# Kernel tuning notes

Measured on AMD Instinct MI355X. Metric: run time of the kernel, lower is better.

## Reference

```python
import jax, jax.numpy as jnp
import numpy as np

N_USERS = 50000
N_ENT = 150000
N = N_USERS + N_ENT
E = 2000000
B = 8192
DIMS = [64, 64, 32, 16]  # emb_dim + weight_size


def _xavier(k, shape):
    fi, fo = (shape[0], shape[1]) if len(shape) == 2 else (1, shape[-1])
    lim = float(np.sqrt(6.0 / (fi + fo)))
    return jax.random.uniform(k, shape, jnp.float32, -lim, lim)


def setup_inputs() -> dict:
    key = jax.random.key(0)
    ks = jax.random.split(key, 32)
    inp = {}
    inp["users"] = jax.random.randint(ks[0], (B,), 0, N_USERS)
    inp["pos_items"] = jax.random.randint(ks[1], (B,), 0, N_ENT)
    inp["neg_items"] = jax.random.randint(ks[2], (B,), 0, N_ENT)
    inp["rows"] = jax.random.randint(ks[3], (E,), 0, N)
    inp["cols"] = jax.random.randint(ks[4], (E,), 0, N)
    # attentive normalized adjacency values (softmax-normalized in KGAT, ~1/degree scale)
    inp["edge_vals"] = jax.random.uniform(ks[5], (E,), jnp.float32) / 10.0
    inp["user_embed"] = _xavier(ks[6], (N_USERS, DIMS[0]))
    inp["entity_embed"] = _xavier(ks[7], (N_ENT, DIMS[0]))
    i = 8
    for l in range(3):
        din, dout = DIMS[l], DIMS[l + 1]
        inp[f"W_gc{l}"] = _xavier(ks[i], (din, dout)); i += 1
        inp[f"b_gc{l}"] = _xavier(ks[i], (1, dout)); i += 1
        inp[f"W_bi{l}"] = _xavier(ks[i], (din, dout)); i += 1
        inp[f"b_bi{l}"] = _xavier(ks[i], (1, dout)); i += 1
    return inp


def _l2norm(x):
    # F.normalize(x, p=2, dim=1)
    return x / jnp.maximum(jnp.linalg.norm(x, axis=1, keepdims=True), 1e-12)


def reference(users, pos_items, neg_items, rows, cols, edge_vals, user_embed, entity_embed,
              W_gc0, b_gc0, W_bi0, b_bi0, W_gc1, b_gc1, W_bi1, b_bi1, W_gc2, b_gc2, W_bi2, b_bi2):
    ego = jnp.concatenate([user_embed, entity_embed], axis=0)  # [N, 64]
    layer_params = [(W_gc0, b_gc0, W_bi0, b_bi0),
                    (W_gc1, b_gc1, W_bi1, b_bi1),
                    (W_gc2, b_gc2, W_bi2, b_bi2)]
    embs = [ego]
    for Wg, bg, Wb, bb in layer_params:
        # side = A_in @ ego  (sparse COO matmul as gather + segment_sum)
        side = jax.ops.segment_sum(edge_vals[:, None] * ego[cols], rows, num_segments=N)
        sum_emb = jax.nn.leaky_relu((ego + side) @ Wg + bg)  # bi-interaction sum branch
        bi_emb = jax.nn.leaky_relu((ego * side) @ Wb + bb)   # bi-interaction elementwise branch
        ego = sum_emb + bi_emb
        embs.append(_l2norm(ego))
    all_emb = jnp.concatenate(embs, axis=1)  # [N, 64+64+32+16]
    ua, ea = all_emb[:N_USERS], all_emb[N_USERS:]
    u_e = ua[users]
    pos_i_e = ea[pos_items]
    neg_i_e = ea[neg_items]
    pos_scores = jnp.sum(u_e * pos_i_e, axis=1)
    neg_scores = jnp.sum(u_e * neg_i_e, axis=1)
    return jnp.stack([pos_scores, neg_scores], axis=-1)  # [B, 2]
```

## Files before the change

kernel.cpp:

```cpp
#include <hip/hip_runtime.h>

#define N_USERS 50000
#define N_ENT   150000
#define N_NODES 200000
#define NE      2000000
#define BATCH   8192

#define BSHIFT 9
#define BROWS  512
#define NBUK   391
#define EPB    4096
#define PBLK   489
#define T0_BLKS 12500
#define WT_BLKS 52

typedef __attribute__((ext_vector_type(8))) short   bf16x8;
typedef __attribute__((ext_vector_type(4))) float   f32x4;

__device__ __forceinline__ float bf2f(unsigned short b) {
    return __uint_as_float(((unsigned int)b) << 16);
}
__device__ __forceinline__ unsigned short f2bf(float f) {
    unsigned int u = __float_as_uint(f);
    u += 0x7FFF + ((u >> 16) & 1);
    return (unsigned short)(u >> 16);
}

__global__ __launch_bounds__(256) void bhist(const int4* __restrict__ rows4,
                                             int* __restrict__ bcnt) {
    __shared__ int lcnt[NBUK];
    for (int b = threadIdx.x; b < NBUK; b += 256) lcnt[b] = 0;
    __syncthreads();
    const int q0 = blockIdx.x * (EPB / 4);
#pragma unroll
    for (int k = 0; k < 4; ++k) {
        int q = q0 + k * 256 + threadIdx.x;
        if (q < NE / 4) {
            int4 r = rows4[q];
            atomicAdd(&lcnt[r.x >> BSHIFT], 1);
            atomicAdd(&lcnt[r.y >> BSHIFT], 1);
            atomicAdd(&lcnt[r.z >> BSHIFT], 1);
            atomicAdd(&lcnt[r.w >> BSHIFT], 1);
        }
    }
    __syncthreads();
    for (int b = threadIdx.x; b < NBUK; b += 256) {
        int c = lcnt[b];
        if (c) atomicAdd(&bcnt[b], c);
    }
}

__global__ __launch_bounds__(512) void bscan(const int* __restrict__ bcnt,
                                             int* __restrict__ bsc,
                                             int* __restrict__ gcur) {
    __shared__ int buf[512];
    int t = threadIdx.x;
    int v = (t < NBUK) ? bcnt[t] : 0;
    buf[t] = v;
    __syncthreads();
    for (int off = 1; off < 512; off <<= 1) {
        int x = (t >= off) ? buf[t - off] : 0;
        __syncthreads();
        buf[t] += x;
        __syncthreads();
    }
    if (t < NBUK) {
        int excl = buf[t] - v;
        bsc[t]  = excl;
        gcur[t] = excl;
    }
    if (t == NBUK - 1) bsc[NBUK] = buf[t];
}

__global__ __launch_bounds__(256) void part_kernel(const int4* __restrict__ rows4,
                                                   const int4* __restrict__ cols4,
                                                   const float4* __restrict__ vals4,
                                                   int* __restrict__ gcur,
                                                   uint2* __restrict__ part) {
    __shared__ int lcnt[NBUK];
    __shared__ int lbase[NBUK];
    for (int b = threadIdx.x; b < NBUK; b += 256) lcnt[b] = 0;
    __syncthreads();
    const int q0 = blockIdx.x * (EPB / 4);
    int4 rc[4];
#pragma unroll
    for (int k = 0; k < 4; ++k) {
        int q = q0 + k * 256 + threadIdx.x;
        if (q < NE / 4) {
            int4 r = rows4[q];
            rc[k] = r;
            atomicAdd(&lcnt[r.x >> BSHIFT], 1);
            atomicAdd(&lcnt[r.y >> BSHIFT], 1);
            atomicAdd(&lcnt[r.z >> BSHIFT], 1);
            atomicAdd(&lcnt[r.w >> BSHIFT], 1);
        } else {
            rc[k] = make_int4(-1, -1, -1, -1);
        }
    }
    __syncthreads();
    for (int b = threadIdx.x; b < NBUK; b += 256) {
        int c = lcnt[b];
        lbase[b] = c ? atomicAdd(&gcur[b], c) : 0;
        lcnt[b] = 0;
    }
    __syncthreads();
#pragma unroll
    for (int k = 0; k < 4; ++k) {
        int q = q0 + k * 256 + threadIdx.x;
        if (q < NE / 4) {
            int4   c4 = cols4[q];
            float4 v4 = vals4[q];
            int r, b, rk;
            uint2 rec;
            r = rc[k].x; b = r >> BSHIFT; rk = atomicAdd(&lcnt[b], 1);
            rec.x = ((unsigned)(r & (BROWS - 1)) << 18) | (unsigned)c4.x;
            rec.y = __float_as_uint(v4.x);  part[lbase[b] + rk] = rec;
            r = rc[k].y; b = r >> BSHIFT; rk = atomicAdd(&lcnt[b], 1);
            rec.x = ((unsigned)(r & (BROWS - 1)) << 18) | (unsigned)c4.y;
            rec.y = __float_as_uint(v4.y);  part[lbase[b] + rk] = rec;
            r = rc[k].z; b = r >> BSHIFT; rk = atomicAdd(&lcnt[b], 1);
            rec.x = ((unsigned)(r & (BROWS - 1)) << 18) | (unsigned)c4.z;
            rec.y = __float_as_uint(v4.z);  part[lbase[b] + rk] = rec;
            r = rc[k].w; b = r >> BSHIFT; rk = atomicAdd(&lcnt[b], 1);
            rec.x = ((unsigned)(r & (BROWS - 1)) << 18) | (unsigned)c4.w;
            rec.y = __float_as_uint(v4.w);  part[lbase[b] + rk] = rec;
        }
    }
}

__global__ __launch_bounds__(512) void bfill(const uint2* __restrict__ part,
                                             const int* __restrict__ bsc,
                                             int* __restrict__ rs,
                                             int* __restrict__ deg,
                                             uint2* __restrict__ ep) {
    __shared__ int h[BROWS];
    __shared__ int sc[BROWS];
    const int b = blockIdx.x;
    const int t = threadIdx.x;
    const int s = bsc[b];
    const int e = bsc[b + 1];
    h[t] = 0;
    __syncthreads();
    for (int i = s + t; i < e; i += 512)
        atomicAdd(&h[part[i].x >> 18], 1);
    __syncthreads();
    int v = h[t];
    sc[t] = v;
    __syncthreads();
    for (int off = 1; off < 512; off <<= 1) {
        int x = (t >= off) ? sc[t - off] : 0;
        __syncthreads();
        sc[t] += x;
        __syncthreads();
    }
    const int row = b * BROWS + t;
    if (row < N_NODES) {
        deg[row] = v;
        rs[row]  = s + sc[t];
    }
    h[t] = s + sc[t] - v;
    __syncthreads();
    for (int i = s + t; i < e; i += 512) {
        uint2 rec = part[i];
        int lr  = rec.x >> 18;
        int pos = atomicAdd(&h[lr], 1);
        uint2 o;
        o.x = rec.x & 0x3FFFF;
        o.y = rec.y;
        ep[pos] = o;
    }
}

__global__ __launch_bounds__(256) void init_misc(
        const float* __restrict__ ue, const float* __restrict__ ee,
        unsigned short* __restrict__ t0,
        const float* __restrict__ Wg0, const float* __restrict__ Wb0,
        const float* __restrict__ Wg1, const float* __restrict__ Wb1,
        const float* __restrict__ Wg2, const float* __restrict__ Wb2,
        unsigned short* __restrict__ wt) {
    if (blockIdx.x < T0_BLKS) {
        int i = blockIdx.x * 256 + threadIdx.x;
        const int uelems = N_USERS * 64 / 4;
        float4 v = (i < uelems) ? ((const float4*)ue)[i]
                                : ((const float4*)ee)[i - uelems];
        ushort4 o;
        o.x = f2bf(v.x); o.y = f2bf(v.y); o.z = f2bf(v.z); o.w = f2bf(v.w);
        ((ushort4*)t0)[i] = o;
        return;
    }
    int idx = (blockIdx.x - T0_BLKS) * 256 + threadIdx.x;
    if (idx < 4096) {
        int k = idx >> 6, n = idx & 63;
        wt[0 + n * 64 + k] = f2bf(Wg0[idx]);
    } else if (idx < 8192) {
        int r = idx - 4096; int k = r >> 6, n = r & 63;
        wt[4096 + n * 64 + k] = f2bf(Wb0[r]);
    } else if (idx < 10240) {
        int r = idx - 8192; int k = r >> 5, n = r & 31;
        wt[8192 + n * 64 + k] = f2bf(Wg1[r]);
    } else if (idx < 12288) {
        int r = idx - 10240; int k = r >> 5, n = r & 31;
        wt[10240 + n * 64 + k] = f2bf(Wb1[r]);
    } else if (idx < 12800) {
        int r = idx - 12288; int k = r >> 4, n = r & 15;
        wt[12288 + n * 32 + k] = f2bf(Wg2[r]);
    } else if (idx < 13312) {
        int r = idx - 12800; int k = r >> 4, n = r & 15;
        wt[12800 + n * 32 + k] = f2bf(Wb2[r]);
    }
}

template <int DIN, int DOUT, int EGO, int WX>
__global__ __launch_bounds__(256) void layer_fused(
        const int* __restrict__ rs, const int* __restrict__ deg,
        const uint2* __restrict__ ep,
        const unsigned short* __restrict__ tin,
        const float* __restrict__ ue, const float* __restrict__ ee,
        const float* __restrict__ xin,
        const unsigned short* __restrict__ WgT,
        const unsigned short* __restrict__ WbT,
        const float* __restrict__ bg, const float* __restrict__ bb,
        float* __restrict__ xout,
        unsigned short* __restrict__ tout,
        float* __restrict__ norm_out) {
    constexpr int NTC = DOUT / 16;
    constexpr int R   = (4 / NTC) * 16;
    constexpr int RPW = R / 4;
    constexpr int KS  = DIN / 32;

    __shared__ unsigned short sH[R * DIN];
    __shared__ unsigned short sP[R * DIN];
    __shared__ float sPart[R * NTC];

    const int lane    = threadIdx.x & 63;
    const int wave    = threadIdx.x >> 6;
    const int rowbase = blockIdx.x * R;

    for (int rr = 0; rr < RPW; ++rr) {
        const int lr  = wave * RPW + rr;
        const int row = __builtin_amdgcn_readfirstlane(rowbase + lr);
        const int end   = rs[row];
        const int start = end - deg[row];

        float acc;
        if (DIN == 64) {
            float a0 = 0.f, a1 = 0.f, a2 = 0.f, a3 = 0.f;
            for (int i = start; i < end; i += 4) {
                uint2 r0 = ep[i + 0], r1 = ep[i + 1];
                uint2 r2 = ep[i + 2], r3 = ep[i + 3];
                int c0 = (int)r0.x;
                int c1 = ((unsigned)r1.x < N_NODES) ? (int)r1.x : 0;
                int c2 = ((unsigned)r2.x < N_NODES) ? (int)r2.x : 0;
                int c3 = ((unsigned)r3.x < N_NODES) ? (int)r3.x : 0;
                float v0 = __uint_as_float(r0.y);
                float v1 = (i + 1 < end) ? __uint_as_float(r1.y) : 0.f;
                float v2 = (i + 2 < end) ? __uint_as_float(r2.y) : 0.f;
                float v3 = (i + 3 < end) ? __uint_as_float(r3.y) : 0.f;
                a0 = fmaf(v0, bf2f(tin[(size_t)c0 * 64 + lane]), a0);
                a1 = fmaf(v1, bf2f(tin[(size_t)c1 * 64 + lane]), a1);
                a2 = fmaf(v2, bf2f(tin[(size_t)c2 * 64 + lane]), a2);
                a3 = fmaf(v3, bf2f(tin[(size_t)c3 * 64 + lane]), a3);
            }
            acc = (a0 + a1) + (a2 + a3);
        } else {
            const int g = lane >> 5;
            const int d = lane & 31;
            float a0 = 0.f, a1 = 0.f, a2 = 0.f, a3 = 0.f;
            for (int i = start; i < end; i += 8) {
                uint2 r0 = ep[i + 0], r1 = ep[i + 1], r2 = ep[i + 2], r3 = ep[i + 3];
                uint2 r4 = ep[i + 4], r5 = ep[i + 5], r6 = ep[i + 6], r7 = ep[i + 7];
                int c0 = (int)r0.x;
                int c1 = ((unsigned)r1.x < N_NODES) ? (int)r1.x : 0;
                int c2 = ((unsigned)r2.x < N_NODES) ? (int)r2.x : 0;
                int c3 = ((unsigned)r3.x < N_NODES) ? (int)r3.x : 0;
                int c4 = ((unsigned)r4.x < N_NODES) ? (int)r4.x : 0;
                int c5 = ((unsigned)r5.x < N_NODES) ? (int)r5.x : 0;
                int c6 = ((unsigned)r6.x < N_NODES) ? (int)r6.x : 0;
                int c7 = ((unsigned)r7.x < N_NODES) ? (int)r7.x : 0;
                float v0 = __uint_as_float(r0.y);
                float v1 = (i + 1 < end) ? __uint_as_float(r1.y) : 0.f;
                float v2 = (i + 2 < end) ? __uint_as_float(r2.y) : 0.f;
                float v3 = (i + 3 < end) ? __uint_as_float(r3.y) : 0.f;
                float v4 = (i + 4 < end) ? __uint_as_float(r4.y) : 0.f;
                float v5 = (i + 5 < end) ? __uint_as_float(r5.y) : 0.f;
                float v6 = (i + 6 < end) ? __uint_as_float(r6.y) : 0.f;
                float v7 = (i + 7 < end) ? __uint_as_float(r7.y) : 0.f;
                int   ca = g ? c4 : c0;  float va = g ? v4 : v0;
                int   cb = g ? c5 : c1;  float vb = g ? v5 : v1;
                int   cc = g ? c6 : c2;  float vc = g ? v6 : v2;
                int   cd = g ? c7 : c3;  float vd = g ? v7 : v3;
                a0 = fmaf(va, bf2f(tin[(size_t)ca * 32 + d]), a0);
                a1 = fmaf(vb, bf2f(tin[(size_t)cb * 32 + d]), a1);
                a2 = fmaf(vc, bf2f(tin[(size_t)cc * 32 + d]), a2);
                a3 = fmaf(vd, bf2f(tin[(size_t)cd * 32 + d]), a3);
            }
            acc = (a0 + a1) + (a2 + a3);
            acc += __shfl_xor(acc, 32);
        }

        const int d = (DIN == 64) ? lane : (lane & 31);
        float e;
        if (EGO == 0) {
            e = (row < N_USERS) ? ue[(size_t)row * 64 + lane]
                                : ee[(size_t)(row - N_USERS) * 64 + lane];
        } else if (EGO == 1) {
            e = xin[(size_t)row * DIN + lane];
        } else {
            e = bf2f(tin[(size_t)row * DIN + d]);
        }
        float h = e + acc;
        float p = e * acc;
        if (DIN == 64 || lane < 32) {
            sH[lr * DIN + d] = f2bf(h);
            sP[lr * DIN + d] = f2bf(p);
        }
    }
    __syncthreads();

    const int ct  = wave % NTC;
    const int rt  = wave / NTC;
    const int r16 = lane & 15;
    const int g4  = lane >> 4;

    bf16x8 ah[KS], ap[KS];
#pragma unroll
    for (int s = 0; s < KS; ++s) {
        const int aoff = (rt * 16 + r16) * DIN + g4 * 8 + s * 32;
        ah[s] = *reinterpret_cast<const bf16x8*>(sH + aoff);
        ap[s] = *reinterpret_cast<const bf16x8*>(sP + aoff);
    }
    f32x4 accg = (f32x4){0.f, 0.f, 0.f, 0.f};
    f32x4 accb = (f32x4){0.f, 0.f, 0.f, 0.f};
#pragma unroll
    for (int s = 0; s < KS; ++s) {
        const int boff = (ct * 16 + r16) * DIN + g4 * 8 + s * 32;
        bf16x8 bgf = *reinterpret_cast<const bf16x8*>(WgT + boff);
        bf16x8 bbf = *reinterpret_cast<const bf16x8*>(WbT + boff);
        accg = __builtin_amdgcn_mfma_f32_16x16x32_bf16(ah[s], bgf, accg, 0, 0, 0);
        accb = __builtin_amdgcn_mfma_f32_16x16x32_bf16(ap[s], bbf, accb, 0, 0, 0);
    }

    const int col = ct * 16 + r16;
    const float bgv = bg[col];
    const float bbv = bb[col];
    float ss[4];
#pragma unroll
    for (int r = 0; r < 4; ++r) {
        float a = accg[r] + bgv; a = a > 0.f ? a : 0.01f * a;
        float b = accb[r] + bbv; b = b > 0.f ? b : 0.01f * b;
        float nv = a + b;
        const int row = rowbase + rt * 16 + g4 * 4 + r;
        if (WX) xout[(size_t)row * DOUT + col] = nv;
        tout[(size_t)row * DOUT + col] = f2bf(nv);
        ss[r] = nv * nv;
    }
#pragma unroll
    for (int off = 1; off < 16; off <<= 1) {
#pragma unroll
        for (int r = 0; r < 4; ++r) ss[r] += __shfl_xor(ss[r], off);
    }
    if (r16 == 0) {
#pragma unroll
        for (int r = 0; r < 4; ++r)
            sPart[(rt * 16 + g4 * 4 + r) * NTC + ct] = ss[r];
    }
    __syncthreads();
    for (int t = threadIdx.x; t < R; t += 256) {
        float s = 0.f;
#pragma unroll
        for (int j = 0; j < NTC; ++j) s += sPart[t * NTC + j];
        norm_out[rowbase + t] = fmaxf(sqrtf(s), 1e-12f);
    }
}

__global__ __launch_bounds__(256) void score_kernel(
        const int* __restrict__ users, const int* __restrict__ pos,
        const int* __restrict__ neg,
        const float* __restrict__ ue, const float* __restrict__ ee,
        const float* __restrict__ e1, const float* __restrict__ n0,
        const unsigned short* __restrict__ t2, const float* __restrict__ n1,
        const unsigned short* __restrict__ t3, const float* __restrict__ n2,
        float* __restrict__ out) {
    int gid  = blockIdx.x * 256 + threadIdx.x;
    int idx  = gid >> 6;
    int lane = gid & 63;
    if (idx >= BATCH) return;
    int u  = users[idx];
    int pe = pos[idx];
    int ne = neg[idx];
    int pn = N_USERS + pe;
    int nn = N_USERS + ne;

    float s1p = 1.0f / (n0[u] * n0[pn]);
    float s1n = 1.0f / (n0[u] * n0[nn]);
    float s2p = 1.0f / (n1[u] * n1[pn]);
    float s2n = 1.0f / (n1[u] * n1[nn]);
    float s3p = 1.0f / (n2[u] * n2[pn]);
    float s3n = 1.0f / (n2[u] * n2[nn]);

    float ap = 0.f, an = 0.f;
    {
        float xu = ue[(size_t)u * 64 + lane];
        ap += xu * ee[(size_t)pe * 64 + lane];
        an += xu * ee[(size_t)ne * 64 + lane];
    }
    {
        float xu = e1[(size_t)u * 64 + lane];
        ap += xu * e1[(size_t)pn * 64 + lane] * s1p;
        an += xu * e1[(size_t)nn * 64 + lane] * s1n;
    }
    if (lane < 32) {
        float xu = bf2f(t2[(size_t)u * 32 + lane]);
        ap += xu * bf2f(t2[(size_t)pn * 32 + lane]) * s2p;
        an += xu * bf2f(t2[(size_t)nn * 32 + lane]) * s2n;
    } else if (lane < 48) {
        int d = lane - 32;
        float xu = bf2f(t3[(size_t)u * 16 + d]);
        ap += xu * bf2f(t3[(size_t)pn * 16 + d]) * s3p;
        an += xu * bf2f(t3[(size_t)nn * 16 + d]) * s3n;
    }
#pragma unroll
    for (int off = 32; off > 0; off >>= 1) {
        ap += __shfl_xor(ap, off);
        an += __shfl_xor(an, off);
    }
    if (lane == 0) {
        out[2 * idx + 0] = ap;
        out[2 * idx + 1] = an;
    }
}

extern "C" void kernel_launch(void* const* d_in, const int* in_sizes, int n_in,
                              void* d_out, int out_size, void* d_ws, size_t ws_size,
                              hipStream_t stream) {
    const int*   users = (const int*)d_in[0];
    const int*   pos   = (const int*)d_in[1];
    const int*   neg   = (const int*)d_in[2];
    const int*   rows  = (const int*)d_in[3];
    const int*   cols  = (const int*)d_in[4];
    const float* vals  = (const float*)d_in[5];
    const float* ue    = (const float*)d_in[6];
    const float* ee    = (const float*)d_in[7];
    const float* Wg0 = (const float*)d_in[8],  *bg0 = (const float*)d_in[9];
    const float* Wb0 = (const float*)d_in[10], *bb0 = (const float*)d_in[11];
    const float* Wg1 = (const float*)d_in[12], *bg1 = (const float*)d_in[13];
    const float* Wb1 = (const float*)d_in[14], *bb1 = (const float*)d_in[15];
    const float* Wg2 = (const float*)d_in[16], *bg2 = (const float*)d_in[17];
    const float* Wb2 = (const float*)d_in[18], *bb2 = (const float*)d_in[19];

    float* e1   = (float*)d_ws;
    float* n0   = e1 + (size_t)N_NODES * 64;
    float* n1   = n0 + N_NODES;
    float* n2   = n1 + N_NODES;
    uint2* ep   = (uint2*)(n2 + N_NODES);
    unsigned short* tA = (unsigned short*)(ep + NE);
    unsigned short* tB = tA + (size_t)N_NODES * 64;
    unsigned short* t3 = tB + (size_t)N_NODES * 64;
    unsigned short* wt = t3 + (size_t)N_NODES * 16;
    int* deg  = (int*)(wt + 13312);
    int* rs   = deg + N_NODES;
    int* bcnt = rs + N_NODES;
    int* bsc  = bcnt + NBUK;
    int* gcur = bsc + NBUK + 1;
    uint2* part = (uint2*)e1;

    hipMemsetAsync(bcnt, 0, NBUK * sizeof(int), stream);
    bhist<<<PBLK, 256, 0, stream>>>((const int4*)rows, bcnt);
    bscan<<<1, 512, 0, stream>>>(bcnt, bsc, gcur);
    part_kernel<<<PBLK, 256, 0, stream>>>((const int4*)rows, (const int4*)cols,
                                          (const float4*)vals, gcur, part);
    bfill<<<NBUK, 512, 0, stream>>>(part, bsc, rs, deg, ep);
    init_misc<<<T0_BLKS + WT_BLKS, 256, 0, stream>>>(ue, ee, tA,
                                                     Wg0, Wb0, Wg1, Wb1, Wg2, Wb2, wt);

    layer_fused<64, 64, 0, 1><<<N_NODES / 16, 256, 0, stream>>>(
        rs, deg, ep, tA, ue, ee, nullptr, wt, wt + 4096, bg0, bb0, e1, tB, n0);
    layer_fused<64, 32, 1, 0><<<N_NODES / 32, 256, 0, stream>>>(
        rs, deg, ep, tB, ue, ee, e1, wt + 8192, wt + 10240, bg1, bb1, nullptr, tA, n1);
    layer_fused<32, 16, 2, 0><<<N_NODES / 64, 256, 0, stream>>>(
        rs, deg, ep, tA, ue, ee, nullptr, wt + 12288, wt + 12800, bg2, bb2, nullptr, t3, n2);

    score_kernel<<<(BATCH * 64) / 256, 256, 0, stream>>>(users, pos, neg, ue, ee,
                                                         e1, n0, tA, n1, t3, n2,
                                                         (float*)d_out);
}
```

Baseline: 474.1 us.

## Gather two bf16 features per lane and process more edges per wave in SpMM

The SpMM gather in the fused layer kernel now loads packed pairs of bf16 features as 32-bit words. This lets a 64-wide row be covered by half a wave and a 32-wide row by a quarter wave, so each wave works on more edges at once. The partial sums are then combined with cross-lane shuffles. The partitioning kernels also handle twice as many edges per block, with half as many blocks, to cut atomic and launch overhead. In exchange the inner loop needs more shuffles and lane-select logic, and the larger partition blocks may lower occupancy.

```diff
diff --git a/kernel.cpp b/kernel.cpp
--- a/kernel.cpp
+++ b/kernel.cpp
@@ -9,19 +9,26 @@
 #define BSHIFT 9
 #define BROWS  512
 #define NBUK   391
-#define EPB    4096
-#define PBLK   489
+#define EPB    8192
+#define PBLK   245
 #define T0_BLKS 12500
 #define WT_BLKS 52
 
 typedef __attribute__((ext_vector_type(8))) short   bf16x8;
 typedef __attribute__((ext_vector_type(4))) float   f32x4;
+typedef unsigned int u32;
 
 __device__ __forceinline__ float bf2f(unsigned short b) {
-    return __uint_as_float(((unsigned int)b) << 16);
+    return __uint_as_float(((u32)b) << 16);
+}
+__device__ __forceinline__ float bflo(u32 x) {
+    return __uint_as_float(x << 16);
+}
+__device__ __forceinline__ float bfhi(u32 x) {
+    return __uint_as_float(x & 0xFFFF0000u);
 }
 __device__ __forceinline__ unsigned short f2bf(float f) {
-    unsigned int u = __float_as_uint(f);
+    u32 u = __float_as_uint(f);
     u += 0x7FFF + ((u >> 16) & 1);
     return (unsigned short)(u >> 16);
 }
@@ -33,7 +40,7 @@
     __syncthreads();
     const int q0 = blockIdx.x * (EPB / 4);
 #pragma unroll
-    for (int k = 0; k < 4; ++k) {
+    for (int k = 0; k < EPB / 1024; ++k) {
         int q = q0 + k * 256 + threadIdx.x;
         if (q < NE / 4) {
             int4 r = rows4[q];
@@ -82,9 +89,9 @@
     for (int b = threadIdx.x; b < NBUK; b += 256) lcnt[b] = 0;
     __syncthreads();
     const int q0 = blockIdx.x * (EPB / 4);
-    int4 rc[4];
-#pragma unroll
-    for (int k = 0; k < 4; ++k) {
+    int4 rc[EPB / 1024];
+#pragma unroll
+    for (int k = 0; k < EPB / 1024; ++k) {
         int q = q0 + k * 256 + threadIdx.x;
         if (q < NE / 4) {
             int4 r = rows4[q];
@@ -105,7 +112,7 @@
     }
     __syncthreads();
 #pragma unroll
-    for (int k = 0; k < 4; ++k) {
+    for (int k = 0; k < EPB / 1024; ++k) {
         int q = q0 + k * 256 + threadIdx.x;
         if (q < NE / 4) {
             int4   c4 = cols4[q];
@@ -113,16 +120,16 @@
             int r, b, rk;
             uint2 rec;
             r = rc[k].x; b = r >> BSHIFT; rk = atomicAdd(&lcnt[b], 1);
-            rec.x = ((unsigned)(r & (BROWS - 1)) << 18) | (unsigned)c4.x;
+            rec.x = ((u32)(r & (BROWS - 1)) << 18) | (u32)c4.x;
             rec.y = __float_as_uint(v4.x);  part[lbase[b] + rk] = rec;
             r = rc[k].y; b = r >> BSHIFT; rk = atomicAdd(&lcnt[b], 1);
-            rec.x = ((unsigned)(r & (BROWS - 1)) << 18) | (unsigned)c4.y;
+            rec.x = ((u32)(r & (BROWS - 1)) << 18) | (u32)c4.y;
             rec.y = __float_as_uint(v4.y);  part[lbase[b] + rk] = rec;
             r = rc[k].z; b = r >> BSHIFT; rk = atomicAdd(&lcnt[b], 1);
-            rec.x = ((unsigned)(r & (BROWS - 1)) << 18) | (unsigned)c4.z;
+            rec.x = ((u32)(r & (BROWS - 1)) << 18) | (u32)c4.z;
             rec.y = __float_as_uint(v4.z);  part[lbase[b] + rk] = rec;
             r = rc[k].w; b = r >> BSHIFT; rk = atomicAdd(&lcnt[b], 1);
-            rec.x = ((unsigned)(r & (BROWS - 1)) << 18) | (unsigned)c4.w;
+            rec.x = ((u32)(r & (BROWS - 1)) << 18) | (u32)c4.w;
             rec.y = __float_as_uint(v4.w);  part[lbase[b] + rk] = rec;
         }
     }
@@ -228,8 +235,8 @@
     constexpr int RPW = R / 4;
     constexpr int KS  = DIN / 32;
 
-    __shared__ unsigned short sH[R * DIN];
-    __shared__ unsigned short sP[R * DIN];
+    __shared__ __align__(16) unsigned short sH[R * DIN];
+    __shared__ __align__(16) unsigned short sP[R * DIN];
     __shared__ float sPart[R * NTC];
 
     const int lane    = threadIdx.x & 63;
@@ -242,41 +249,23 @@
         const int end   = rs[row];
         const int start = end - deg[row];
 
-        float acc;
         if (DIN == 64) {
-            float a0 = 0.f, a1 = 0.f, a2 = 0.f, a3 = 0.f;
-            for (int i = start; i < end; i += 4) {
-                uint2 r0 = ep[i + 0], r1 = ep[i + 1];
-                uint2 r2 = ep[i + 2], r3 = ep[i + 3];
-                int c0 = (int)r0.x;
-                int c1 = ((unsigned)r1.x < N_NODES) ? (int)r1.x : 0;
-                int c2 = ((unsigned)r2.x < N_NODES) ? (int)r2.x : 0;
-                int c3 = ((unsigned)r3.x < N_NODES) ? (int)r3.x : 0;
-                float v0 = __uint_as_float(r0.y);
-                float v1 = (i + 1 < end) ? __uint_as_float(r1.y) : 0.f;
-                float v2 = (i + 2 < end) ? __uint_as_float(r2.y) : 0.f;
-                float v3 = (i + 3 < end) ? __uint_as_float(r3.y) : 0.f;
-                a0 = fmaf(v0, bf2f(tin[(size_t)c0 * 64 + lane]), a0);
-                a1 = fmaf(v1, bf2f(tin[(size_t)c1 * 64 + lane]), a1);
-                a2 = fmaf(v2, bf2f(tin[(size_t)c2 * 64 + lane]), a2);
-                a3 = fmaf(v3, bf2f(tin[(size_t)c3 * 64 + lane]), a3);
-            }
-            acc = (a0 + a1) + (a2 + a3);
-        } else {
-            const int g = lane >> 5;
-            const int d = lane & 31;
-            float a0 = 0.f, a1 = 0.f, a2 = 0.f, a3 = 0.f;
+            const int g  = lane >> 5;
+            const int d2 = lane & 31;
+            const u32* t32 = (const u32*)tin;
+            float ax0 = 0.f, ay0 = 0.f, ax1 = 0.f, ay1 = 0.f;
+            float ax2 = 0.f, ay2 = 0.f, ax3 = 0.f, ay3 = 0.f;
             for (int i = start; i < end; i += 8) {
                 uint2 r0 = ep[i + 0], r1 = ep[i + 1], r2 = ep[i + 2], r3 = ep[i + 3];
                 uint2 r4 = ep[i + 4], r5 = ep[i + 5], r6 = ep[i + 6], r7 = ep[i + 7];
                 int c0 = (int)r0.x;
-                int c1 = ((unsigned)r1.x < N_NODES) ? (int)r1.x : 0;
-                int c2 = ((unsigned)r2.x < N_NODES) ? (int)r2.x : 0;
-                int c3 = ((unsigned)r3.x < N_NODES) ? (int)r3.x : 0;
-                int c4 = ((unsigned)r4.x < N_NODES) ? (int)r4.x : 0;
-                int c5 = ((unsigned)r5.x < N_NODES) ? (int)r5.x : 0;
-                int c6 = ((unsigned)r6.x < N_NODES) ? (int)r6.x : 0;
-                int c7 = ((unsigned)r7.x < N_NODES) ? (int)r7.x : 0;
+                int c1 = ((u32)r1.x < N_NODES) ? (int)r1.x : 0;
+                int c2 = ((u32)r2.x < N_NODES) ? (int)r2.x : 0;
+                int c3 = ((u32)r3.x < N_NODES) ? (int)r3.x : 0;
+                int c4 = ((u32)r4.x < N_NODES) ? (int)r4.x : 0;
+                int c5 = ((u32)r5.x < N_NODES) ? (int)r5.x : 0;
+                int c6 = ((u32)r6.x < N_NODES) ? (int)r6.x : 0;
+                int c7 = ((u32)r7.x < N_NODES) ? (int)r7.x : 0;
                 float v0 = __uint_as_float(r0.y);
                 float v1 = (i + 1 < end) ? __uint_as_float(r1.y) : 0.f;
                 float v2 = (i + 2 < end) ? __uint_as_float(r2.y) : 0.f;
@@ -285,34 +274,100 @@
                 float v5 = (i + 5 < end) ? __uint_as_float(r5.y) : 0.f;
                 float v6 = (i + 6 < end) ? __uint_as_float(r6.y) : 0.f;
                 float v7 = (i + 7 < end) ? __uint_as_float(r7.y) : 0.f;
-                int   ca = g ? c4 : c0;  float va = g ? v4 : v0;
-                int   cb = g ? c5 : c1;  float vb = g ? v5 : v1;
-                int   cc = g ? c6 : c2;  float vc = g ? v6 : v2;
-                int   cd = g ? c7 : c3;  float vd = g ? v7 : v3;
-                a0 = fmaf(va, bf2f(tin[(size_t)ca * 32 + d]), a0);
-                a1 = fmaf(vb, bf2f(tin[(size_t)cb * 32 + d]), a1);
-                a2 = fmaf(vc, bf2f(tin[(size_t)cc * 32 + d]), a2);
-                a3 = fmaf(vd, bf2f(tin[(size_t)cd * 32 + d]), a3);
+                int   cA = g ? c1 : c0;  float vA = g ? v1 : v0;
+                int   cB = g ? c3 : c2;  float vB = g ? v3 : v2;
+                int   cC = g ? c5 : c4;  float vC = g ? v5 : v4;
+                int   cD = g ? c7 : c6;  float vD = g ? v7 : v6;
+                u32 xA = t32[(size_t)cA * 32 + d2];
+                u32 xB = t32[(size_t)cB * 32 + d2];
+                u32 xC = t32[(size_t)cC * 32 + d2];
+                u32 xD = t32[(size_t)cD * 32 + d2];
+                ax0 = fmaf(vA, bflo(xA), ax0);  ay0 = fmaf(vA, bfhi(xA), ay0);
+                ax1 = fmaf(vB, bflo(xB), ax1);  ay1 = fmaf(vB, bfhi(xB), ay1);
+                ax2 = fmaf(vC, bflo(xC), ax2);  ay2 = fmaf(vC, bfhi(xC), ay2);
+                ax3 = fmaf(vD, bflo(xD), ax3);  ay3 = fmaf(vD, bfhi(xD), ay3);
             }
-            acc = (a0 + a1) + (a2 + a3);
-            acc += __shfl_xor(acc, 32);
-        }
-
-        const int d = (DIN == 64) ? lane : (lane & 31);
-        float e;
-        if (EGO == 0) {
-            e = (row < N_USERS) ? ue[(size_t)row * 64 + lane]
-                                : ee[(size_t)(row - N_USERS) * 64 + lane];
-        } else if (EGO == 1) {
-            e = xin[(size_t)row * DIN + lane];
+            float ax = (ax0 + ax1) + (ax2 + ax3);
+            float ay = (ay0 + ay1) + (ay2 + ay3);
+            ax += __shfl_xor(ax, 32);
+            ay += __shfl_xor(ay, 32);
+
+            float ex, ey;
+            if (EGO == 0) {
+                const float2* src = (row < N_USERS)
+                    ? (const float2*)ue + (size_t)row * 32
+                    : (const float2*)ee + (size_t)(row - N_USERS) * 32;
+                float2 ev = src[d2];  ex = ev.x;  ey = ev.y;
+            } else if (EGO == 1) {
+                float2 ev = ((const float2*)xin)[(size_t)row * 32 + d2];
+                ex = ev.x;  ey = ev.y;
+            } else {
+                u32 tv = t32[(size_t)row * 32 + d2];
+                ex = bflo(tv);  ey = bfhi(tv);
+            }
+            if (g == 0) {
+                u32 hw = ((u32)f2bf(ey + ay) << 16) | f2bf(ex + ax);
+                u32 pw = ((u32)f2bf(ey * ay) << 16) | f2bf(ex * ax);
+                ((u32*)sH)[lr * 32 + d2] = hw;
+                ((u32*)sP)[lr * 32 + d2] = pw;
+            }
         } else {
-            e = bf2f(tin[(size_t)row * DIN + d]);
-        }
-        float h = e + acc;
-        float p = e * acc;
-        if (DIN == 64 || lane < 32) {
-            sH[lr * DIN + d] = f2bf(h);
-            sP[lr * DIN + d] = f2bf(p);
+            const int g  = lane >> 4;
+            const int d2 = lane & 15;
+            const u32* t16 = (const u32*)tin;
+            float ax0 = 0.f, ay0 = 0.f, ax1 = 0.f, ay1 = 0.f;
+            for (int i = start; i < end; i += 8) {
+                uint2 r0 = ep[i + 0], r1 = ep[i + 1], r2 = ep[i + 2], r3 = ep[i + 3];
+                uint2 r4 = ep[i + 4], r5 = ep[i + 5], r6 = ep[i + 6], r7 = ep[i + 7];
+                int c0 = (int)r0.x;
+                int c1 = ((u32)r1.x < N_NODES) ? (int)r1.x : 0;
+                int c2 = ((u32)r2.x < N_NODES) ? (int)r2.x : 0;
+                int c3 = ((u32)r3.x < N_NODES) ? (int)r3.x : 0;
+                int c4 = ((u32)r4.x < N_NODES) ? (int)r4.x : 0;
+                int c5 = ((u32)r5.x < N_NODES) ? (int)r5.x : 0;
+                int c6 = ((u32)r6.x < N_NODES) ? (int)r6.x : 0;
+                int c7 = ((u32)r7.x < N_NODES) ? (int)r7.x : 0;
+                float v0 = __uint_as_float(r0.y);
+                float v1 = (i + 1 < end) ? __uint_as_float(r1.y) : 0.f;
+                float v2 = (i + 2 < end) ? __uint_as_float(r2.y) : 0.f;
+                float v3 = (i + 3 < end) ? __uint_as_float(r3.y) : 0.f;
+                float v4 = (i + 4 < end) ? __uint_as_float(r4.y) : 0.f;
+                float v5 = (i + 5 < end) ? __uint_as_float(r5.y) : 0.f;
+                float v6 = (i + 6 < end) ? __uint_as_float(r6.y) : 0.f;
+                float v7 = (i + 7 < end) ? __uint_as_float(r7.y) : 0.f;
+                int   cA = (g & 2) ? ((g & 1) ? c3 : c2) : ((g & 1) ? c1 : c0);
+                float vA = (g & 2) ? ((g & 1) ? v3 : v2) : ((g & 1) ? v1 : v0);
+                int   cB = (g & 2) ? ((g & 1) ? c7 : c6) : ((g & 1) ? c5 : c4);
+                float vB = (g & 2) ? ((g & 1) ? v7 : v6) : ((g & 1) ? v5 : v4);
+                u32 xA = t16[(size_t)cA * 16 + d2];
+                u32 xB = t16[(size_t)cB * 16 + d2];
+                ax0 = fmaf(vA, bflo(xA), ax0);  ay0 = fmaf(vA, bfhi(xA), ay0);
+                ax1 = fmaf(vB, bflo(xB), ax1);  ay1 = fmaf(vB, bfhi(xB), ay1);
+            }
+            float ax = ax0 + ax1;
+            float ay = ay0 + ay1;
+            ax += __shfl_xor(ax, 32);  ay += __shfl_xor(ay, 32);
+            ax += __shfl_xor(ax, 16);  ay += __shfl_xor(ay, 16);
+
+            float ex, ey;
+            if (EGO == 2) {
+                u32 tv = t16[(size_t)row * 16 + d2];
+                ex = bflo(tv);  ey = bfhi(tv);
+            } else if (EGO == 1) {
+                float2 ev = ((const float2*)xin)[(size_t)row * 16 + d2];
+                ex = ev.x;  ey = ev.y;
+            } else {
+                const float2* src = (row < N_USERS)
+                    ? (const float2*)ue + (size_t)row * 32
+                    : (const float2*)ee + (size_t)(row - N_USERS) * 32;
+                float2 ev = src[d2];  ex = ev.x;  ey = ev.y;
+            }
+            if (g == 0) {
+                u32 hw = ((u32)f2bf(ey + ay) << 16) | f2bf(ex + ax);
+                u32 pw = ((u32)f2bf(ey * ay) << 16) | f2bf(ex * ax);
+                ((u32*)sH)[lr * 16 + d2] = hw;
+                ((u32*)sP)[lr * 16 + d2] = pw;
+            }
         }
     }
     __syncthreads();
```

After: 442.1 us. 1.07x faster.
